# Kernel tuning notes

Hardware: AMD Instinct MI355X
Metric: run time of the kernel (lower is better)

The kernel has to match this reference:

```python
import jax, jax.numpy as jnp
import numpy as np

GN_GROUPS = 16
GN_EPS = 1e-5
MP_K = 4
CLAMP_MIN, CLAMP_MAX = 0.0, 1.0


def setup_inputs() -> dict:
    key = jax.random.key(0)
    k1, k2, k3, k4 = jax.random.split(key, 4)
    B, Ci, H, W = 128, 8, 128, 128
    Co, K = 64, 3
    return {
        "x": jax.random.normal(k1, (B, Ci, H, W), dtype=jnp.float32),
        "conv_weight": jax.random.normal(k2, (Co, Ci, K, K), dtype=jnp.float32) * 0.1,
        "conv_bias": jax.random.normal(k3, (Co,), dtype=jnp.float32) * 0.1,
        "gn_weight": jnp.ones((Co,), dtype=jnp.float32),
        "gn_bias": jnp.zeros((Co,), dtype=jnp.float32),
        "scale": jax.random.normal(k4, (Co, 1, 1), dtype=jnp.float32),
    }


def reference(x, conv_weight, conv_bias, gn_weight, gn_bias, scale):
    # Conv2d: stride 1, padding 0 (PyTorch defaults) -> [B, Co, H-2, W-2]
    y = jax.lax.conv_general_dilated(
        x, conv_weight, window_strides=(1, 1), padding="VALID",
        dimension_numbers=("NCHW", "OIHW", "NCHW"))
    y = y + conv_bias[None, :, None, None]

    # GroupNorm over (C//G, H, W) per (batch, group)
    B, C, Ho, Wo = y.shape
    yg = y.reshape(B, GN_GROUPS, -1)
    mean = yg.mean(axis=-1, keepdims=True)
    var = yg.var(axis=-1, keepdims=True)
    yn = ((yg - mean) * jax.lax.rsqrt(var + GN_EPS)).reshape(B, C, Ho, Wo)
    yn = yn * gn_weight[None, :, None, None] + gn_bias[None, :, None, None]

    # Scale (broadcast [C,1,1])
    yn = yn * scale[None]

    # MaxPool2d(kernel=4, stride=4, padding=0)
    pooled = jax.lax.reduce_window(
        yn, -jnp.inf, jax.lax.max,
        window_dimensions=(1, 1, MP_K, MP_K),
        window_strides=(1, 1, MP_K, MP_K),
        padding="VALID")

    return jnp.clip(pooled, CLAMP_MIN, CLAMP_MAX)
```

## Files before the change

### kernel.cpp

```cpp
#include <hip/hip_runtime.h>


constexpr int CI   = 8;
constexpr int CO   = 64;
constexpr int HIN  = 128;
constexpr int WIN_ = 128;
constexpr int HO_  = 126;
constexpr int WO_  = 126;
constexpr int CPG  = 4;
constexpr int PW   = 31;
constexpr float EPS = 1e-5f;

__global__ __launch_bounds__(256, 2)
void fused_conv_gn_pool(const float* __restrict__ x,
                        const float* __restrict__ cw,
                        const float* __restrict__ cb,
                        const float* __restrict__ gnw,
                        const float* __restrict__ gnb,
                        const float* __restrict__ scl,
                        float* __restrict__ out)
{
    __shared__ float xb[6][CI][WIN_];
    __shared__ float wl[CI][3][3][CPG];
    __shared__ float rmax[4][CPG][PW];
    __shared__ float rmin[4][CPG][PW];
    __shared__ float wmaxs[CPG][PW][PW];
    __shared__ float wmins[CPG][PW][PW];
    __shared__ float redbuf[4][2];
    __shared__ float statbuf[2];

    const int t   = threadIdx.x;
    const int bid = blockIdx.x;
    const int b   = bid >> 4;
    const int g   = bid & 15;
    const int co0 = g * CPG;

    for (int i = t; i < CI * 9 * CPG; i += 256) {
        int c    = i & 3;
        int rest = i >> 2;
        int kw   = rest % 3;
        int kh   = (rest / 3) % 3;
        int ci   = rest / 9;
        wl[ci][kh][kw][c] = cw[((co0 + c) * CI + ci) * 9 + kh * 3 + kw];
    }

    float bb[CPG];
    #pragma unroll
    for (int c = 0; c < CPG; ++c) bb[c] = cb[co0 + c];

    const int col  = t & 127;
    const int half = t >> 7;
    const float* xbase = x + (size_t)b * CI * HIN * WIN_;

    float s1 = 0.f, s2 = 0.f;

    for (int j = 0; j < 32; ++j) {
        const int r0    = (j == 0) ? 0 : 4 * j + 2;
        const int nload = (j == 0) ? 6 : ((4 * j + 6 <= 128) ? 4 : (128 - r0));
        __syncthreads();
        for (int i = t; i < nload * CI * WIN_; i += 256) {
            int cc = i & 127;
            int ci = (i >> 7) & 7;
            int rr = i >> 10;
            int gr = r0 + rr;
            xb[gr % 6][ci][cc] = xbase[(ci * HIN + gr) * WIN_ + cc];
        }
        __syncthreads();

        const int orow = 4 * j + 2 * half;
        if (orow < HO_ && col < WO_) {
            float a0[CPG] = {0.f, 0.f, 0.f, 0.f};
            float a1[CPG] = {0.f, 0.f, 0.f, 0.f};
            int sl[4];
            {
                int sb = orow % 6;
                #pragma unroll
                for (int ir = 0; ir < 4; ++ir) {
                    int s = sb + ir;
                    sl[ir] = (s >= 6) ? s - 6 : s;
                }
            }
            for (int ci = 0; ci < CI; ++ci) {
                float xv[4][3];
                #pragma unroll
                for (int ir = 0; ir < 4; ++ir) {
                    xv[ir][0] = xb[sl[ir]][ci][col];
                    xv[ir][1] = xb[sl[ir]][ci][col + 1];
                    xv[ir][2] = xb[sl[ir]][ci][col + 2];
                }
                #pragma unroll
                for (int kh = 0; kh < 3; ++kh)
                #pragma unroll
                for (int kw = 0; kw < 3; ++kw) {
                    #pragma unroll
                    for (int c = 0; c < CPG; ++c) {
                        float w = wl[ci][kh][kw][c];
                        a0[c] = fmaf(w, xv[kh][kw], a0[c]);
                        a1[c] = fmaf(w, xv[kh + 1][kw], a1[c]);
                    }
                }
            }
            #pragma unroll
            for (int c = 0; c < CPG; ++c) {
                a0[c] += bb[c];
                a1[c] += bb[c];
                s1 += a0[c] + a1[c];
                s2 += a0[c] * a0[c] + a1[c] * a1[c];
            }
            if (j < 31) {
                #pragma unroll
                for (int c = 0; c < CPG; ++c) {
                    float m0 = fmaxf(a0[c], __shfl_xor(a0[c], 1));
                    m0       = fmaxf(m0,   __shfl_xor(m0, 2));
                    float n0 = fminf(a0[c], __shfl_xor(a0[c], 1));
                    n0       = fminf(n0,   __shfl_xor(n0, 2));
                    float m1 = fmaxf(a1[c], __shfl_xor(a1[c], 1));
                    m1       = fmaxf(m1,   __shfl_xor(m1, 2));
                    float n1 = fminf(a1[c], __shfl_xor(a1[c], 1));
                    n1       = fminf(n1,   __shfl_xor(n1, 2));
                    if ((col & 3) == 0 && col < 124) {
                        int pj = col >> 2;
                        rmax[2 * half + 0][c][pj] = m0;
                        rmin[2 * half + 0][c][pj] = n0;
                        rmax[2 * half + 1][c][pj] = m1;
                        rmin[2 * half + 1][c][pj] = n1;
                    }
                }
            }
        }
        __syncthreads();
        if (j < 31 && t < CPG * PW) {
            int c  = t / PW;
            int pj = t - c * PW;
            float M = fmaxf(fmaxf(rmax[0][c][pj], rmax[1][c][pj]),
                            fmaxf(rmax[2][c][pj], rmax[3][c][pj]));
            float N = fminf(fminf(rmin[0][c][pj], rmin[1][c][pj]),
                            fminf(rmin[2][c][pj], rmin[3][c][pj]));
            wmaxs[c][j][pj] = M;
            wmins[c][j][pj] = N;
        }
    }

    #pragma unroll
    for (int off = 1; off < 64; off <<= 1) {
        s1 += __shfl_xor(s1, off);
        s2 += __shfl_xor(s2, off);
    }
    if ((t & 63) == 0) {
        redbuf[t >> 6][0] = s1;
        redbuf[t >> 6][1] = s2;
    }
    __syncthreads();
    if (t == 0) {
        float S1 = 0.f, S2 = 0.f;
        #pragma unroll
        for (int w = 0; w < 4; ++w) { S1 += redbuf[w][0]; S2 += redbuf[w][1]; }
        const float invN = 1.0f / (float)(CPG * HO_ * WO_);
        float mean = S1 * invN;
        float var  = S2 * invN - mean * mean;
        statbuf[0] = mean;
        statbuf[1] = rsqrtf(var + EPS);
    }
    __syncthreads();
    const float mean = statbuf[0];
    const float inv  = statbuf[1];

    for (int i = t; i < CPG * PW * PW; i += 256) {
        int c   = i / (PW * PW);
        int rem = i - c * PW * PW;
        int pi  = rem / PW;
        int pj  = rem - pi * PW;
        int co  = co0 + c;
        float A = inv * gnw[co] * scl[co];
        float B = (gnb[co] - mean * inv * gnw[co]) * scl[co];
        float v = (A > 0.f) ? fmaf(A, wmaxs[c][pi][pj], B)
                            : fmaf(A, wmins[c][pi][pj], B);
        v = fminf(fmaxf(v, 0.f), 1.f);
        out[(((size_t)b * CO + co) * PW + pi) * PW + pj] = v;
    }
}

extern "C" void kernel_launch(void* const* d_in, const int* in_sizes, int n_in,
                              void* d_out, int out_size, void* d_ws, size_t ws_size,
                              hipStream_t stream) {
    const float* x   = (const float*)d_in[0];
    const float* cw  = (const float*)d_in[1];
    const float* cb  = (const float*)d_in[2];
    const float* gnw = (const float*)d_in[3];
    const float* gnb = (const float*)d_in[4];
    const float* scl = (const float*)d_in[5];
    float* out = (float*)d_out;

    fused_conv_gn_pool<<<dim3(128 * 16), dim3(256), 0, stream>>>(
        x, cw, cb, gnw, gnb, scl, out);
}
```

Measured before the change: 549.1 us.

## Register-block conv per thread over 4 columns and pick pool extreme by sign

Each thread now computes one output channel over a 2x4 output tile, with its 72 weights held in registers instead of read from shared memory. Input rows are loaded as float4 and the conv reads its window through vector LDS loads. The pooling step keeps only the max or the min, chosen up front from the sign of gnw*scale, and reduces it with a single shuffle. This drops the separate max/min reduction pass and one block barrier per row step. Register pressure rises (a 72-float weight array plus a 4x6 input tile) while launch bounds ask for 3 blocks per CU, so spills or occupancy limits are a risk.

```diff
diff --git a/kernel.cpp b/kernel.cpp
--- a/kernel.cpp
+++ b/kernel.cpp
@@ -6,12 +6,11 @@
 constexpr int HIN  = 128;
 constexpr int WIN_ = 128;
 constexpr int HO_  = 126;
-constexpr int WO_  = 126;
 constexpr int CPG  = 4;
 constexpr int PW   = 31;
 constexpr float EPS = 1e-5f;
 
-__global__ __launch_bounds__(256, 2)
+__global__ __launch_bounds__(256, 3)
 void fused_conv_gn_pool(const float* __restrict__ x,
                         const float* __restrict__ cw,
                         const float* __restrict__ cb,
@@ -21,123 +20,107 @@
                         float* __restrict__ out)
 {
     __shared__ float xb[6][CI][WIN_];
-    __shared__ float wl[CI][3][3][CPG];
-    __shared__ float rmax[4][CPG][PW];
-    __shared__ float rmin[4][CPG][PW];
-    __shared__ float wmaxs[CPG][PW][PW];
-    __shared__ float wmins[CPG][PW][PW];
+    __shared__ float wpool[CPG][PW][PW];
     __shared__ float redbuf[4][2];
     __shared__ float statbuf[2];
 
     const int t   = threadIdx.x;
-    const int bid = blockIdx.x;
-    const int b   = bid >> 4;
-    const int g   = bid & 15;
+    const int b   = blockIdx.x >> 4;
+    const int g   = blockIdx.x & 15;
     const int co0 = g * CPG;
 
-    for (int i = t; i < CI * 9 * CPG; i += 256) {
-        int c    = i & 3;
-        int rest = i >> 2;
-        int kw   = rest % 3;
-        int kh   = (rest / 3) % 3;
-        int ci   = rest / 9;
-        wl[ci][kh][kw][c] = cw[((co0 + c) * CI + ci) * 9 + kh * 3 + kw];
+    const int c    = t & 3;
+    const int rh   = (t >> 2) & 1;
+    const int cg   = t >> 3;
+    const int col0 = cg * 4;
+    const int co   = co0 + c;
+
+    float w[72];
+    {
+        const float4* wp4 = (const float4*)(cw + (size_t)co * (CI * 9));
+        #pragma unroll
+        for (int i = 0; i < 18; ++i) ((float4*)w)[i] = wp4[i];
     }
+    const float bias = cb[co];
+    const bool  pos  = (gnw[co] * scl[co] >= 0.f);
 
-    float bb[CPG];
-    #pragma unroll
-    for (int c = 0; c < CPG; ++c) bb[c] = cb[co0 + c];
-
-    const int col  = t & 127;
-    const int half = t >> 7;
     const float* xbase = x + (size_t)b * CI * HIN * WIN_;
 
     float s1 = 0.f, s2 = 0.f;
 
     for (int j = 0; j < 32; ++j) {
-        const int r0    = (j == 0) ? 0 : 4 * j + 2;
-        const int nload = (j == 0) ? 6 : ((4 * j + 6 <= 128) ? 4 : (128 - r0));
         __syncthreads();
-        for (int i = t; i < nload * CI * WIN_; i += 256) {
-            int cc = i & 127;
-            int ci = (i >> 7) & 7;
-            int rr = i >> 10;
-            int gr = r0 + rr;
-            xb[gr % 6][ci][cc] = xbase[(ci * HIN + gr) * WIN_ + cc];
+        if (j == 0) {
+            for (int k = t; k < 6 * CI * 32; k += 256) {
+                int cc4 = k & 31, ci = (k >> 5) & 7, rr = k >> 8;
+                ((float4*)&xb[rr][ci][0])[cc4] =
+                    ((const float4*)(xbase + (ci * HIN + rr) * WIN_))[cc4];
+            }
+        } else {
+            const int r0    = 4 * j + 2;
+            const int nrows = (j < 31) ? 4 : 2;
+            for (int k = t; k < nrows * CI * 32; k += 256) {
+                int cc4 = k & 31, ci = (k >> 5) & 7, rr = k >> 8;
+                int gr  = r0 + rr;
+                ((float4*)&xb[gr % 6][ci][0])[cc4] =
+                    ((const float4*)(xbase + (ci * HIN + gr) * WIN_))[cc4];
+            }
         }
         __syncthreads();
 
-        const int orow = 4 * j + 2 * half;
-        if (orow < HO_ && col < WO_) {
-            float a0[CPG] = {0.f, 0.f, 0.f, 0.f};
-            float a1[CPG] = {0.f, 0.f, 0.f, 0.f};
+        const int r0h = 4 * j + 2 * rh;
+        if (r0h < HO_) {
+            float acc[2][4] = {{0.f,0.f,0.f,0.f},{0.f,0.f,0.f,0.f}};
             int sl[4];
-            {
-                int sb = orow % 6;
+            #pragma unroll
+            for (int kr = 0; kr < 4; ++kr) sl[kr] = (r0h + kr) % 6;
+
+            #pragma unroll
+            for (int ci = 0; ci < CI; ++ci) {
+                float xv[4][6];
                 #pragma unroll
-                for (int ir = 0; ir < 4; ++ir) {
-                    int s = sb + ir;
-                    sl[ir] = (s >= 6) ? s - 6 : s;
-                }
-            }
-            for (int ci = 0; ci < CI; ++ci) {
-                float xv[4][3];
-                #pragma unroll
-                for (int ir = 0; ir < 4; ++ir) {
-                    xv[ir][0] = xb[sl[ir]][ci][col];
-                    xv[ir][1] = xb[sl[ir]][ci][col + 1];
-                    xv[ir][2] = xb[sl[ir]][ci][col + 2];
+                for (int kr = 0; kr < 4; ++kr) {
+                    float4 v4 = *(const float4*)&xb[sl[kr]][ci][col0];
+                    xv[kr][0] = v4.x; xv[kr][1] = v4.y;
+                    xv[kr][2] = v4.z; xv[kr][3] = v4.w;
+                    float2 v2 = *(const float2*)&xb[sl[kr]][ci][col0 + 4];
+                    xv[kr][4] = v2.x; xv[kr][5] = v2.y;
                 }
                 #pragma unroll
                 for (int kh = 0; kh < 3; ++kh)
                 #pragma unroll
                 for (int kw = 0; kw < 3; ++kw) {
+                    float wv = w[ci * 9 + kh * 3 + kw];
                     #pragma unroll
-                    for (int c = 0; c < CPG; ++c) {
-                        float w = wl[ci][kh][kw][c];
-                        a0[c] = fmaf(w, xv[kh][kw], a0[c]);
-                        a1[c] = fmaf(w, xv[kh + 1][kw], a1[c]);
+                    for (int q = 0; q < 4; ++q) {
+                        acc[0][q] = fmaf(wv, xv[kh][kw + q],     acc[0][q]);
+                        acc[1][q] = fmaf(wv, xv[kh + 1][kw + q], acc[1][q]);
                     }
                 }
             }
+
             #pragma unroll
-            for (int c = 0; c < CPG; ++c) {
-                a0[c] += bb[c];
-                a1[c] += bb[c];
-                s1 += a0[c] + a1[c];
-                s2 += a0[c] * a0[c] + a1[c] * a1[c];
+            for (int r = 0; r < 2; ++r)
+            #pragma unroll
+            for (int q = 0; q < 4; ++q) {
+                float v = acc[r][q] + bias;
+                acc[r][q] = v;
+                if ((cg < 31) | (q < 2)) { s1 += v; s2 = fmaf(v, v, s2); }
             }
-            if (j < 31) {
-                #pragma unroll
-                for (int c = 0; c < CPG; ++c) {
-                    float m0 = fmaxf(a0[c], __shfl_xor(a0[c], 1));
-                    m0       = fmaxf(m0,   __shfl_xor(m0, 2));
-                    float n0 = fminf(a0[c], __shfl_xor(a0[c], 1));
-                    n0       = fminf(n0,   __shfl_xor(n0, 2));
-                    float m1 = fmaxf(a1[c], __shfl_xor(a1[c], 1));
-                    m1       = fmaxf(m1,   __shfl_xor(m1, 2));
-                    float n1 = fminf(a1[c], __shfl_xor(a1[c], 1));
-                    n1       = fminf(n1,   __shfl_xor(n1, 2));
-                    if ((col & 3) == 0 && col < 124) {
-                        int pj = col >> 2;
-                        rmax[2 * half + 0][c][pj] = m0;
-                        rmin[2 * half + 0][c][pj] = n0;
-                        rmax[2 * half + 1][c][pj] = m1;
-                        rmin[2 * half + 1][c][pj] = n1;
-                    }
+
+            if (j < PW) {
+                float e;
+                if (pos) {
+                    e = fmaxf(fmaxf(fmaxf(acc[0][0], acc[0][1]), fmaxf(acc[0][2], acc[0][3])),
+                              fmaxf(fmaxf(acc[1][0], acc[1][1]), fmaxf(acc[1][2], acc[1][3])));
+                    e = fmaxf(e, __shfl_xor(e, 4));
+                } else {
+                    e = fminf(fminf(fminf(acc[0][0], acc[0][1]), fminf(acc[0][2], acc[0][3])),
+                              fminf(fminf(acc[1][0], acc[1][1]), fminf(acc[1][2], acc[1][3])));
+                    e = fminf(e, __shfl_xor(e, 4));
                 }
+                if (rh == 0 && cg < PW) wpool[c][j][cg] = e;
             }
-        }
-        __syncthreads();
-        if (j < 31 && t < CPG * PW) {
-            int c  = t / PW;
-            int pj = t - c * PW;
-            float M = fmaxf(fmaxf(rmax[0][c][pj], rmax[1][c][pj]),
-                            fmaxf(rmax[2][c][pj], rmax[3][c][pj]));
-            float N = fminf(fminf(rmin[0][c][pj], rmin[1][c][pj]),
-                            fminf(rmin[2][c][pj], rmin[3][c][pj]));
-            wmaxs[c][j][pj] = M;
-            wmins[c][j][pj] = N;
         }
     }
 
@@ -146,16 +129,13 @@
         s1 += __shfl_xor(s1, off);
         s2 += __shfl_xor(s2, off);
     }
-    if ((t & 63) == 0) {
-        redbuf[t >> 6][0] = s1;
-        redbuf[t >> 6][1] = s2;
-    }
+    if ((t & 63) == 0) { redbuf[t >> 6][0] = s1; redbuf[t >> 6][1] = s2; }
     __syncthreads();
     if (t == 0) {
         float S1 = 0.f, S2 = 0.f;
         #pragma unroll
-        for (int w = 0; w < 4; ++w) { S1 += redbuf[w][0]; S2 += redbuf[w][1]; }
-        const float invN = 1.0f / (float)(CPG * HO_ * WO_);
+        for (int wv = 0; wv < 4; ++wv) { S1 += redbuf[wv][0]; S2 += redbuf[wv][1]; }
+        const float invN = 1.0f / (float)(CPG * HO_ * HO_);
         float mean = S1 * invN;
         float var  = S2 * invN - mean * mean;
         statbuf[0] = mean;
@@ -166,17 +146,16 @@
     const float inv  = statbuf[1];
 
     for (int i = t; i < CPG * PW * PW; i += 256) {
-        int c   = i / (PW * PW);
-        int rem = i - c * PW * PW;
+        int cc  = i / (PW * PW);
+        int rem = i - cc * (PW * PW);
         int pi  = rem / PW;
         int pj  = rem - pi * PW;
-        int co  = co0 + c;
-        float A = inv * gnw[co] * scl[co];
-        float B = (gnb[co] - mean * inv * gnw[co]) * scl[co];
-        float v = (A > 0.f) ? fmaf(A, wmaxs[c][pi][pj], B)
-                            : fmaf(A, wmins[c][pi][pj], B);
+        int cox = co0 + cc;
+        float A  = inv * gnw[cox] * scl[cox];
+        float Bv = (gnb[cox] - mean * inv * gnw[cox]) * scl[cox];
+        float v  = fmaf(A, wpool[cc][pi][pj], Bv);
         v = fminf(fmaxf(v, 0.f), 1.f);
-        out[(((size_t)b * CO + co) * PW + pi) * PW + pj] = v;
+        out[(((size_t)b * CO + cox) * PW + pi) * PW + pj] = v;
     }
 }
 
@@ -190,6 +169,7 @@
     const float* gnb = (const float*)d_in[4];
     const float* scl = (const float*)d_in[5];
     float* out = (float*)d_out;
+    (void)d_ws; (void)ws_size; (void)in_sizes; (void)n_in; (void)out_size;
 
     fused_conv_gn_pool<<<dim3(128 * 16), dim3(256), 0, stream>>>(
         x, cw, cb, gnw, gnb, scl, out);
```

New measurement: 715.8 us. 1.3x slower.
